# Performance work log

Measured on AMD Instinct MI355X. Metric: run time of the kernel, lower is better.

The kernel has to match this reference:

```python
import jax, jax.numpy as jnp
import numpy as np

EMBED_DIM = 1024
NUM_HEADS = 16
HEAD_DIM = EMBED_DIM // NUM_HEADS
B, S = 4, 2048


def setup_inputs() -> dict:
    key = jax.random.key(0)
    ks = jax.random.split(key, 9)
    scale = 1.0 / np.sqrt(EMBED_DIM)
    x = jax.random.normal(ks[0], (B, S, EMBED_DIM), dtype=jnp.float32)
    Wq = jax.random.uniform(ks[1], (EMBED_DIM, EMBED_DIM), jnp.float32, -scale, scale)
    bq = jax.random.uniform(ks[2], (EMBED_DIM,), jnp.float32, -scale, scale)
    Wk = jax.random.uniform(ks[3], (EMBED_DIM, EMBED_DIM), jnp.float32, -scale, scale)
    bk = jax.random.uniform(ks[4], (EMBED_DIM,), jnp.float32, -scale, scale)
    Wv = jax.random.uniform(ks[5], (EMBED_DIM, EMBED_DIM), jnp.float32, -scale, scale)
    bv = jax.random.uniform(ks[6], (EMBED_DIM,), jnp.float32, -scale, scale)
    Wo = jax.random.uniform(ks[7], (EMBED_DIM, EMBED_DIM), jnp.float32, -scale, scale)
    bo = jax.random.uniform(ks[8], (EMBED_DIM,), jnp.float32, -scale, scale)
    return {"x": x, "Wq": Wq, "bq": bq, "Wk": Wk, "bk": bk, "Wv": Wv, "bv": bv, "Wo": Wo, "bo": bo}


def reference(x, Wq, bq, Wk, bk, Wv, bv, Wo, bo):
    b, s, d = x.shape
    h, hd = NUM_HEADS, HEAD_DIM
    # projections -> [b, h, s, hd]
    def proj(W, bias):
        return (x @ W + bias).reshape(b, s, h, hd).transpose(0, 2, 1, 3)
    q = proj(Wq, bq)
    k = proj(Wk, bk)
    v = proj(Wv, bv)
    logits = jnp.einsum('bhqd,bhkd->bhqk', q, k) / np.sqrt(hd).astype(np.float32)
    attn = jax.nn.softmax(logits, axis=-1)  # dropout p=0.0 -> identity
    vals = jnp.einsum('bhqk,bhkd->bhqd', attn, v)
    vals = vals.transpose(0, 2, 1, 3).reshape(b, s, d)
    return vals @ Wo + bo
```

## Files before the change

### kernel.cpp

```cpp
#include <hip/hip_runtime.h>

typedef unsigned short u16;
typedef unsigned int u32;
typedef __bf16 bf16x8 __attribute__((ext_vector_type(8)));
typedef float f32x4 __attribute__((ext_vector_type(4)));
typedef float f32x16 __attribute__((ext_vector_type(16)));
typedef u32 u32x4 __attribute__((ext_vector_type(4)));
typedef u32 u32x2 __attribute__((ext_vector_type(2)));

#define NBATCH 4
#define NS 2048
#define ND 1024
#define NH 16
#define HDIM 64
#define KSCALE (0.125f * 1.44269504f)

#define MFMA(a, b, c) __builtin_amdgcn_mfma_f32_16x16x32_bf16(a, b, c, 0, 0, 0)
#define MFMA32(a, b, c) __builtin_amdgcn_mfma_f32_32x32x16_bf16(a, b, c, 0, 0, 0)

__device__ __forceinline__ u16 f2bf(float f) {
    u32 u = __builtin_bit_cast(u32, f);
    u += 0x7fffu + ((u >> 16) & 1u);
    return (u16)(u >> 16);
}

__device__ __forceinline__ u32 cvtpk(float a, float b) {
    u32 r;
    asm("v_cvt_pk_bf16_f32 %0, %1, %2" : "=v"(r) : "v"(a), "v"(b));
    return r;
}

__device__ __forceinline__ bf16x8 ldfrag(const u16* p) {
    u32x4 v = *(const u32x4*)p;
    return __builtin_bit_cast(bf16x8, v);
}

__device__ __forceinline__ void gld16(u16* lds, const u16* g) {
    __builtin_amdgcn_global_load_lds((__attribute__((address_space(1))) u32*)g,
                                     (__attribute__((address_space(3))) u32*)lds, 16, 0, 0);
}


__global__ __launch_bounds__(256) void prep(const float* __restrict__ x, const float* __restrict__ W0,
                                            const float* __restrict__ W1, const float* __restrict__ W2,
                                            const float* __restrict__ W3, u16* __restrict__ xb,
                                            u16* __restrict__ T0, u16* __restrict__ T1,
                                            u16* __restrict__ T2, u16* __restrict__ T3) {
    __shared__ u16 t[64][72];
    const int wg = blockIdx.x;
    const int tid = threadIdx.x;
    if (wg < 2048) {
        const int mt = wg >> 5, ktile = wg & 31;
        u16* out = xb + (size_t)wg * 4096;
#pragma unroll
        for (int half = 0; half < 2; ++half) {
            const int s = half * 256 + tid;
            const int rg = s >> 6, l = s & 63;
            const int row = mt * 128 + rg * 16 + (l & 15);
            const int col = ktile * 32 + (l >> 4) * 8;
            const float* sp = x + (size_t)row * ND + col;
            float4 v0 = *(const float4*)sp;
            float4 v1 = *(const float4*)(sp + 4);
            u32x4 o;
            o[0] = (u32)f2bf(v0.x) | ((u32)f2bf(v0.y) << 16);
            o[1] = (u32)f2bf(v0.z) | ((u32)f2bf(v0.w) << 16);
            o[2] = (u32)f2bf(v1.x) | ((u32)f2bf(v1.y) << 16);
            o[3] = (u32)f2bf(v1.z) | ((u32)f2bf(v1.w) << 16);
            *(u32x4*)(out + s * 8) = o;
        }
        return;
    }
    const int tt = wg - 2048;
    const int z = tt >> 8, r8 = tt & 255;
    const float* W = z == 0 ? W0 : z == 1 ? W1 : z == 2 ? W2 : W3;
    u16* WT = z == 0 ? T0 : z == 1 ? T1 : z == 2 ? T2 : T3;
    const int k0 = (r8 & 15) * 64, n0 = (r8 >> 4) * 64;
    {
        const int r = tid >> 2, cq = (tid & 3) * 16;
#pragma unroll
        for (int i = 0; i < 4; ++i) {
            float4 v = *(const float4*)(W + (size_t)(k0 + r) * ND + n0 + cq + i * 4);
            t[r][cq + i * 4 + 0] = f2bf(v.x);
            t[r][cq + i * 4 + 1] = f2bf(v.y);
            t[r][cq + i * 4 + 2] = f2bf(v.z);
            t[r][cq + i * 4 + 3] = f2bf(v.w);
        }
    }
    __syncthreads();
    {
        const int rr = tid >> 2, cq = (tid & 3) * 16;
        u32x4 o0, o1;
#pragma unroll
        for (int j = 0; j < 4; ++j) {
            o0[j] = (u32)t[cq + 2 * j][rr] | ((u32)t[cq + 2 * j + 1][rr] << 16);
            o1[j] = (u32)t[cq + 8 + 2 * j][rr] | ((u32)t[cq + 8 + 2 * j + 1][rr] << 16);
        }
        const int n_g = n0 + rr;
        const int nt = n_g >> 7, rgn = (n_g >> 4) & 7, lr = n_g & 15;
        const int k_g = k0 + cq;
        const int kt2 = k_g >> 5, lg = (k_g >> 3) & 3;
        u16* outb = WT + ((size_t)(nt * 32 + kt2)) * 4096 + rgn * 512 + lr * 8;
        *(u32x4*)(outb + lg * 128) = o0;
        *(u32x4*)(outb + (lg + 1) * 128) = o1;
    }
}

template <bool PF>
__device__ __forceinline__ void gemm_step(const bf16x8 (&a)[4], const bf16x8 (&b)[4],
                                          bf16x8 (&an)[4], bf16x8 (&bn)[4],
                                          const u16* aw, const u16* bw, int kt,
                                          f32x4 (&acc)[4][4]) {
    if (PF) {
        const u16* ap = aw + (size_t)(kt + 1) * 4096;
        const u16* bp = bw + (size_t)(kt + 1) * 4096;
#pragma unroll
        for (int i = 0; i < 4; ++i) {
            an[i] = ldfrag(ap + i * 512);
            bn[i] = ldfrag(bp + i * 512);
        }
    }
    __builtin_amdgcn_s_setprio(1);
#pragma unroll
    for (int mb = 0; mb < 4; ++mb)
#pragma unroll
        for (int nb = 0; nb < 4; ++nb)
            acc[mb][nb] = MFMA(a[mb], b[nb], acc[mb][nb]);
    __builtin_amdgcn_s_setprio(0);
}

__global__ __launch_bounds__(256, 3) void gemm_qkv(const u16* __restrict__ A,
                                                   const u16* __restrict__ wqT, const u16* __restrict__ wkT,
                                                   const u16* __restrict__ wvT,
                                                   const float* __restrict__ bq, const float* __restrict__ bk,
                                                   const float* __restrict__ bv,
                                                   u16* __restrict__ Qp, u16* __restrict__ Kf,
                                                   u16* __restrict__ Vf) {
    const int wg = blockIdx.x;
    const int xcd = wg & 7, idx = wg >> 3;
    const int ybl = xcd * 8 + idx / 24;
    const int xbl = idx % 24;
    const int region = xbl >> 3;
    const int m0 = ybl * 128, n0 = (xbl & 7) * 128;
    const u16* Bt = region == 0 ? wqT : region == 1 ? wkT : wvT;
    const float* bias = region == 0 ? bq : region == 1 ? bk : bv;

    const int tid = threadIdx.x;
    const int l = tid & 63, w = tid >> 6;
    const int lr = l & 15, lg = l >> 4;
    const int wr = w >> 1, wc = w & 1;

    const u16* aw = A + (size_t)ybl * 32 * 4096 + wr * 2048 + l * 8;
    const u16* bw = Bt + (size_t)(xbl & 7) * 32 * 4096 + wc * 2048 + l * 8;

    f32x4 acc[4][4] = {};
    bf16x8 aA[4], bA[4], aB[4], bB[4];
#pragma unroll
    for (int i = 0; i < 4; ++i) {
        aA[i] = ldfrag(aw + i * 512);
        bA[i] = ldfrag(bw + i * 512);
    }

    for (int kt = 0; kt < 32; kt += 2) {
        gemm_step<true>(aA, bA, aB, bB, aw, bw, kt, acc);
        if (kt + 2 < 32)
            gemm_step<true>(aB, bB, aA, bA, aw, bw, kt + 1, acc);
        else
            gemm_step<false>(aB, bB, aA, bA, aw, bw, kt + 1, acc);
    }

#pragma unroll
    for (int mb = 0; mb < 4; ++mb) {
#pragma unroll
        for (int nb = 0; nb < 4; ++nb) {
            const int col = n0 + wc * 64 + nb * 16 + lr;
            const float bia = bias[col];
            const int hd = col & 63, h = col >> 6;
            if (region == 2) {
                const int rowb = m0 + wr * 64 + mb * 16 + lg * 4;
                const int b = rowb >> 11, kv = rowb & 2047;
                const int bh = b * NH + h;
                const int ktp = kv >> 6, ks = (kv >> 4) & 3, hif = (kv >> 3) & 1, j0 = kv & 7;
                const int lane = (hd & 31) | (hif << 5);
                u32x2 o;
                o[0] = (u32)f2bf(acc[mb][nb][0] + bia) | ((u32)f2bf(acc[mb][nb][1] + bia) << 16);
                o[1] = (u32)f2bf(acc[mb][nb][2] + bia) | ((u32)f2bf(acc[mb][nb][3] + bia) << 16);
                size_t off = (size_t)bh * 131072 + (size_t)ktp * 4096 +
                             (size_t)(((ks + 4 * (hd >> 5)) * 64 + lane) * 8 + j0);
                *(u32x2*)(Vf + off) = o;
            } else if (region == 1) {
#pragma unroll
                for (int r = 0; r < 4; ++r) {
                    const int rowg = m0 + wr * 64 + mb * 16 + lg * 4 + r;
                    float v = (acc[mb][nb][r] + bia) * KSCALE;
                    const int b = rowg >> 11, kv = rowg & 2047;
                    const int bh = b * NH + h;
                    const int ktp = kv >> 6, kvb = (kv >> 5) & 1;
                    const int lane = (kv & 31) | (((hd >> 3) & 1) << 5);
                    size_t o = (size_t)bh * 131072 + (size_t)ktp * 4096 +
                               (size_t)(((kvb * 4 + (hd >> 4)) * 64 + lane) * 8 + (hd & 7));
                    Kf[o] = f2bf(v);
                }
            } else {
#pragma unroll
                for (int r = 0; r < 4; ++r) {
                    const int rowg = m0 + wr * 64 + mb * 16 + lg * 4 + r;
                    float v = acc[mb][nb][r] + bia;
                    size_t o = ((size_t)((rowg >> 11) * NH + h) * NS + (rowg & 2047)) * HDIM + hd;
                    Qp[o] = f2bf(v);
                }
            }
        }
    }
}

__global__ __launch_bounds__(256, 3) void gemm_o(const u16* __restrict__ A, const u16* __restrict__ Bt,
                                                 const float* __restrict__ bias, float* __restrict__ of32) {
    const int wg = blockIdx.x;
    const int xcd = wg & 7, idx = wg >> 3;
    const int ybl = xcd * 8 + (idx >> 3);
    const int xbl = idx & 7;
    const int m0 = ybl * 128, n0 = xbl * 128;

    const int tid = threadIdx.x;
    const int l = tid & 63, w = tid >> 6;
    const int lr = l & 15, lg = l >> 4;
    const int wr = w >> 1, wc = w & 1;

    const u16* aw = A + (size_t)ybl * 32 * 4096 + wr * 2048 + l * 8;
    const u16* bw = Bt + (size_t)xbl * 32 * 4096 + wc * 2048 + l * 8;

    f32x4 acc[4][4] = {};
    bf16x8 aA[4], bA[4], aB[4], bB[4];
#pragma unroll
    for (int i = 0; i < 4; ++i) {
        aA[i] = ldfrag(aw + i * 512);
        bA[i] = ldfrag(bw + i * 512);
    }

    for (int kt = 0; kt < 32; kt += 2) {
        gemm_step<true>(aA, bA, aB, bB, aw, bw, kt, acc);
        if (kt + 2 < 32)
            gemm_step<true>(aB, bB, aA, bA, aw, bw, kt + 1, acc);
        else
            gemm_step<false>(aB, bB, aA, bA, aw, bw, kt + 1, acc);
    }

#pragma unroll
    for (int mb = 0; mb < 4; ++mb) {
#pragma unroll
        for (int nb = 0; nb < 4; ++nb) {
            const int col = n0 + wc * 64 + nb * 16 + lr;
            const float bia = bias[col];
#pragma unroll
            for (int r = 0; r < 4; ++r) {
                const int rowg = m0 + wr * 64 + mb * 16 + lg * 4 + r;
                of32[(size_t)rowg * ND + col] = acc[mb][nb][r] + bia;
            }
        }
    }
}

__global__ __launch_bounds__(256, 3) void attn(const u16* __restrict__ Q, const u16* __restrict__ Kf,
                                               const u16* __restrict__ Vf, u16* __restrict__ AO) {
    __shared__ u16 sm[20480];
    const int tid = threadIdx.x;
    const int l = tid & 63, w = tid >> 6;
    const int lq = l & 31, hi = l >> 5;
    const int wg = blockIdx.x;
    const int xcd = wg & 7, idx = wg >> 3;
    const int bh = xcd * 8 + (idx >> 4);
    const int qb = idx & 15;
    const int qbase = qb * 128 + w * 32;

    const u16* Qrow = Q + ((size_t)bh * NS + qbase + lq) * HDIM;
    bf16x8 qf[4];
#pragma unroll
    for (int kh = 0; kh < 4; ++kh) qf[kh] = ldfrag(Qrow + kh * 16 + hi * 8);

    f32x16 oacc[2] = {};
    f32x16 sA[2] = {}, sB[2] = {};
    float ls0 = 0.f, ls1 = 0.f, ls2 = 0.f, ls3 = 0.f;

    const u16* KfB = Kf + (size_t)bh * 131072;
    const u16* VfB = Vf + (size_t)bh * 131072;

    auto finish = [&](f32x16(&prv)[2], const u16* vlb) {
#pragma unroll
        for (int kvb = 0; kvb < 2; ++kvb) {
#pragma unroll
            for (int i = 0; i < 16; i += 4) {
                float p0 = __builtin_amdgcn_exp2f(prv[kvb][i + 0]);
                float p1 = __builtin_amdgcn_exp2f(prv[kvb][i + 1]);
                float p2 = __builtin_amdgcn_exp2f(prv[kvb][i + 2]);
                float p3 = __builtin_amdgcn_exp2f(prv[kvb][i + 3]);
                prv[kvb][i + 0] = p0;
                prv[kvb][i + 1] = p1;
                prv[kvb][i + 2] = p2;
                prv[kvb][i + 3] = p3;
                ls0 += p0;
                ls1 += p1;
                ls2 += p2;
                ls3 += p3;
            }
        }
        bf16x8 pf[4];
#pragma unroll
        for (int ks = 0; ks < 4; ++ks) {
            const int i0 = 2 * ks, i1 = 2 * ks + 1;
            const int q20 = i0 & 3, kvb0 = i0 >> 2;
            const int q21 = i1 & 3, kvb1 = i1 >> 2;
            u32 W00 = cvtpk(prv[kvb0][4 * q20 + 0], prv[kvb0][4 * q20 + 1]);
            u32 W01 = cvtpk(prv[kvb0][4 * q20 + 2], prv[kvb0][4 * q20 + 3]);
            u32 W10 = cvtpk(prv[kvb1][4 * q21 + 0], prv[kvb1][4 * q21 + 1]);
            u32 W11 = cvtpk(prv[kvb1][4 * q21 + 2], prv[kvb1][4 * q21 + 3]);
            u32x2 s0 = __builtin_amdgcn_permlane32_swap(W00, W10, false, false);
            u32x2 s1 = __builtin_amdgcn_permlane32_swap(W01, W11, false, false);
            u32x4 words;
            words[0] = s0[0];
            words[1] = s1[0];
            words[2] = s0[1];
            words[3] = s1[1];
            pf[ks] = __builtin_bit_cast(bf16x8, words);
        }
#pragma unroll
        for (int hdb = 0; hdb < 2; ++hdb) {
            bf16x8 vf[4];
#pragma unroll
            for (int ks = 0; ks < 4; ++ks) vf[ks] = ldfrag(vlb + ((hdb * 4 + ks) * 64 + l) * 8);
            __builtin_amdgcn_s_setprio(1);
#pragma unroll
            for (int ks = 0; ks < 4; ++ks) oacc[hdb] = MFMA32(vf[ks], pf[ks], oacc[hdb]);
            __builtin_amdgcn_s_setprio(0);
        }
    };

    auto body = [&](int t, f32x16(&cur)[2], f32x16(&prv)[2], int dofin, int dostage) {
        if (dostage) {
            const u16* kg = KfB + (size_t)(t + 1) * 4096;
            const u16* vg = VfB + (size_t)(t + 1) * 4096;
            u16* kd = sm + ((t + 1) & 1) * 4096;
            u16* vd = sm + 8192 + ((t + 1) % 3) * 4096;
            gld16(kd + tid * 8, kg + tid * 8);
            gld16(kd + (256 + tid) * 8, kg + (256 + tid) * 8);
            gld16(vd + tid * 8, vg + tid * 8);
            gld16(vd + (256 + tid) * 8, vg + (256 + tid) * 8);
        }
        const u16* klb = sm + (t & 1) * 4096;
        f32x16 zv = {};
        cur[0] = zv;
        cur[1] = zv;
#pragma unroll
        for (int kvb = 0; kvb < 2; ++kvb) {
            bf16x8 kf[4];
#pragma unroll
            for (int kh = 0; kh < 4; ++kh) kf[kh] = ldfrag(klb + ((kvb * 4 + kh) * 64 + l) * 8);
            __builtin_amdgcn_s_setprio(1);
#pragma unroll
            for (int kh = 0; kh < 4; ++kh) cur[kvb] = MFMA32(kf[kh], qf[kh], cur[kvb]);
            __builtin_amdgcn_s_setprio(0);
        }
        if (dofin) finish(prv, sm + 8192 + ((t - 1) % 3) * 4096);
        __syncthreads();
    };

    gld16(sm + tid * 8, KfB + tid * 8);
    gld16(sm + (256 + tid) * 8, KfB + (256 + tid) * 8);
    gld16(sm + 8192 + tid * 8, VfB + tid * 8);
    gld16(sm + 8192 + (256 + tid) * 8, VfB + (256 + tid) * 8);
    __syncthreads();

    body(0, sA, sB, 0, 1);
    for (int t = 1; t < 31; t += 2) {
        body(t, sB, sA, 1, 1);
        body(t + 1, sA, sB, 1, 1);
    }
    body(31, sB, sA, 1, 0);
    finish(sB, sm + 8192 + (31 % 3) * 4096);

    float lsum = (ls0 + ls1) + (ls2 + ls3);
    lsum += __shfl_xor(lsum, 32);

    u16* ot = sm + w * 2048;
    const float inv = 1.f / lsum;
#pragma unroll
    for (int hdb = 0; hdb < 2; ++hdb)
#pragma unroll
        for (int q2 = 0; q2 < 4; ++q2)
#pragma unroll
            for (int rp = 0; rp < 2; ++rp) {
                u32 word = cvtpk(oacc[hdb][4 * q2 + 2 * rp] * inv, oacc[hdb][4 * q2 + 2 * rp + 1] * inv);
                const int hd0 = hdb * 32 + 8 * q2 + 4 * hi + 2 * rp;
                const int byteoff = lq * 128 + ((2 * hd0) ^ ((lq & 7) << 4));
                *(u32*)((char*)ot + byteoff) = word;
            }
    const int b = bh >> 4, h = bh & 15;
#pragma unroll
    for (int p = 0; p < 4; ++p) {
        const int pidx = p * 64 + l;
        const int row = pidx >> 3;
        const int cb = ((pidx & 7) * 16) ^ ((row & 7) << 4);
        u32x4 val = *(u32x4*)((char*)ot + row * 128 + cb);
        const int m = b * NS + qbase + row;
        const int c = h * 64 + (pidx & 7) * 8;
        const int mt = m >> 7, rg = (m >> 4) & 7, lrm = m & 15;
        const int ktile = c >> 5, lgc = (c >> 3) & 3;
        *(u32x4*)(AO + ((size_t)(mt * 32 + ktile)) * 4096 + rg * 512 + (lgc * 16 + lrm) * 8) = val;
    }
}

extern "C" void kernel_launch(void* const* d_in, const int* in_sizes, int n_in,
                              void* d_out, int out_size, void* d_ws, size_t ws_size,
                              hipStream_t stream) {
    const float* x = (const float*)d_in[0];
    const float* Wq = (const float*)d_in[1];
    const float* bq = (const float*)d_in[2];
    const float* Wk = (const float*)d_in[3];
    const float* bk = (const float*)d_in[4];
    const float* Wv = (const float*)d_in[5];
    const float* bv = (const float*)d_in[6];
    const float* Wo = (const float*)d_in[7];
    const float* bo = (const float*)d_in[8];
    float* out = (float*)d_out;

    u16* ws = (u16*)d_ws;
    u16* xb = ws;
    u16* wqT = ws + 8388608;
    u16* wkT = wqT + 1048576;
    u16* wvT = wkT + 1048576;
    u16* woT = wvT + 1048576;
    u16* Qp = woT + 1048576;
    u16* Kfp = Qp + 8388608;
    u16* Vfp = Kfp + 8388608;
    u16* AO = xb;

    prep<<<3072, 256, 0, stream>>>(x, Wq, Wk, Wv, Wo, xb, wqT, wkT, wvT, woT);
    gemm_qkv<<<1536, 256, 0, stream>>>(xb, wqT, wkT, wvT, bq, bk, bv, Qp, Kfp, Vfp);
    attn<<<1024, 256, 0, stream>>>(Qp, Kfp, Vfp, AO);
    gemm_o<<<512, 256, 0, stream>>>(AO, woT, bo, out);
}
```

Measured before the change: 183.5 us.

## Drop cross-tile software pipelining in attention to raise occupancy to 4 waves

Removes the two-stage S/P pipeline, which kept two score-accumulator sets live across KV tiles, and instead computes scores, exp, packing and the PV MFMA within each KV sub-block. V staging shrinks from triple to double buffering, reducing LDS from 40KB to 32KB, and launch bounds rise from 3 to 4 blocks per CU. The aim is to lower register and LDS pressure so more waves can hide latency. The cost is less intra-wave overlap between the exp/convert work and the MFMA work.

Result: no change. 183.5 us (median of 2 runs) (+0.0%).

```diff
diff --git a/kernel.cpp b/kernel.cpp
--- a/kernel.cpp
+++ b/kernel.cpp
@@ -260,9 +260,9 @@
     }
 }
 
-__global__ __launch_bounds__(256, 3) void attn(const u16* __restrict__ Q, const u16* __restrict__ Kf,
+__global__ __launch_bounds__(256, 4) void attn(const u16* __restrict__ Q, const u16* __restrict__ Kf,
                                                const u16* __restrict__ Vf, u16* __restrict__ AO) {
-    __shared__ u16 sm[20480];
+    __shared__ u16 sm[16384];
     const int tid = threadIdx.x;
     const int l = tid & 63, w = tid >> 6;
     const int lq = l & 31, hi = l >> 5;
@@ -278,90 +278,10 @@
     for (int kh = 0; kh < 4; ++kh) qf[kh] = ldfrag(Qrow + kh * 16 + hi * 8);
 
     f32x16 oacc[2] = {};
-    f32x16 sA[2] = {}, sB[2] = {};
     float ls0 = 0.f, ls1 = 0.f, ls2 = 0.f, ls3 = 0.f;
 
     const u16* KfB = Kf + (size_t)bh * 131072;
     const u16* VfB = Vf + (size_t)bh * 131072;
-
-    auto finish = [&](f32x16(&prv)[2], const u16* vlb) {
-#pragma unroll
-        for (int kvb = 0; kvb < 2; ++kvb) {
-#pragma unroll
-            for (int i = 0; i < 16; i += 4) {
-                float p0 = __builtin_amdgcn_exp2f(prv[kvb][i + 0]);
-                float p1 = __builtin_amdgcn_exp2f(prv[kvb][i + 1]);
-                float p2 = __builtin_amdgcn_exp2f(prv[kvb][i + 2]);
-                float p3 = __builtin_amdgcn_exp2f(prv[kvb][i + 3]);
-                prv[kvb][i + 0] = p0;
-                prv[kvb][i + 1] = p1;
-                prv[kvb][i + 2] = p2;
-                prv[kvb][i + 3] = p3;
-                ls0 += p0;
-                ls1 += p1;
-                ls2 += p2;
-                ls3 += p3;
-            }
-        }
-        bf16x8 pf[4];
-#pragma unroll
-        for (int ks = 0; ks < 4; ++ks) {
-            const int i0 = 2 * ks, i1 = 2 * ks + 1;
-            const int q20 = i0 & 3, kvb0 = i0 >> 2;
-            const int q21 = i1 & 3, kvb1 = i1 >> 2;
-            u32 W00 = cvtpk(prv[kvb0][4 * q20 + 0], prv[kvb0][4 * q20 + 1]);
-            u32 W01 = cvtpk(prv[kvb0][4 * q20 + 2], prv[kvb0][4 * q20 + 3]);
-            u32 W10 = cvtpk(prv[kvb1][4 * q21 + 0], prv[kvb1][4 * q21 + 1]);
-            u32 W11 = cvtpk(prv[kvb1][4 * q21 + 2], prv[kvb1][4 * q21 + 3]);
-            u32x2 s0 = __builtin_amdgcn_permlane32_swap(W00, W10, false, false);
-            u32x2 s1 = __builtin_amdgcn_permlane32_swap(W01, W11, false, false);
-            u32x4 words;
-            words[0] = s0[0];
-            words[1] = s1[0];
-            words[2] = s0[1];
-            words[3] = s1[1];
-            pf[ks] = __builtin_bit_cast(bf16x8, words);
-        }
-#pragma unroll
-        for (int hdb = 0; hdb < 2; ++hdb) {
-            bf16x8 vf[4];
-#pragma unroll
-            for (int ks = 0; ks < 4; ++ks) vf[ks] = ldfrag(vlb + ((hdb * 4 + ks) * 64 + l) * 8);
-            __builtin_amdgcn_s_setprio(1);
-#pragma unroll
-            for (int ks = 0; ks < 4; ++ks) oacc[hdb] = MFMA32(vf[ks], pf[ks], oacc[hdb]);
-            __builtin_amdgcn_s_setprio(0);
-        }
-    };
-
-    auto body = [&](int t, f32x16(&cur)[2], f32x16(&prv)[2], int dofin, int dostage) {
-        if (dostage) {
-            const u16* kg = KfB + (size_t)(t + 1) * 4096;
-            const u16* vg = VfB + (size_t)(t + 1) * 4096;
-            u16* kd = sm + ((t + 1) & 1) * 4096;
-            u16* vd = sm + 8192 + ((t + 1) % 3) * 4096;
-            gld16(kd + tid * 8, kg + tid * 8);
-            gld16(kd + (256 + tid) * 8, kg + (256 + tid) * 8);
-            gld16(vd + tid * 8, vg + tid * 8);
-            gld16(vd + (256 + tid) * 8, vg + (256 + tid) * 8);
-        }
-        const u16* klb = sm + (t & 1) * 4096;
-        f32x16 zv = {};
-        cur[0] = zv;
-        cur[1] = zv;
-#pragma unroll
-        for (int kvb = 0; kvb < 2; ++kvb) {
-            bf16x8 kf[4];
-#pragma unroll
-            for (int kh = 0; kh < 4; ++kh) kf[kh] = ldfrag(klb + ((kvb * 4 + kh) * 64 + l) * 8);
-            __builtin_amdgcn_s_setprio(1);
-#pragma unroll
-            for (int kh = 0; kh < 4; ++kh) cur[kvb] = MFMA32(kf[kh], qf[kh], cur[kvb]);
-            __builtin_amdgcn_s_setprio(0);
-        }
-        if (dofin) finish(prv, sm + 8192 + ((t - 1) % 3) * 4096);
-        __syncthreads();
-    };
 
     gld16(sm + tid * 8, KfB + tid * 8);
     gld16(sm + (256 + tid) * 8, KfB + (256 + tid) * 8);
@@ -369,13 +289,93 @@
     gld16(sm + 8192 + (256 + tid) * 8, VfB + (256 + tid) * 8);
     __syncthreads();
 
-    body(0, sA, sB, 0, 1);
-    for (int t = 1; t < 31; t += 2) {
-        body(t, sB, sA, 1, 1);
-        body(t + 1, sA, sB, 1, 1);
-    }
-    body(31, sB, sA, 1, 0);
-    finish(sB, sm + 8192 + (31 % 3) * 4096);
+    for (int kt = 0; kt < 32; ++kt) {
+        const int cur = kt & 1;
+        if (kt < 31) {
+            const u16* kg = KfB + (size_t)(kt + 1) * 4096;
+            const u16* vg = VfB + (size_t)(kt + 1) * 4096;
+            u16* kd = sm + (cur ^ 1) * 4096;
+            u16* vd = sm + 8192 + (cur ^ 1) * 4096;
+            gld16(kd + tid * 8, kg + tid * 8);
+            gld16(kd + (256 + tid) * 8, kg + (256 + tid) * 8);
+            gld16(vd + tid * 8, vg + tid * 8);
+            gld16(vd + (256 + tid) * 8, vg + (256 + tid) * 8);
+        }
+        const u16* klb = sm + cur * 4096;
+        const u16* vlb = sm + 8192 + cur * 4096;
+
+#pragma unroll
+        for (int kvb = 0; kvb < 2; ++kvb) {
+            bf16x8 kf[4];
+#pragma unroll
+            for (int kh = 0; kh < 4; ++kh)
+                kf[kh] = ldfrag(klb + ((kvb * 4 + kh) * 64 + l) * 8);
+
+            f32x16 sacc = {};
+            __builtin_amdgcn_s_setprio(1);
+#pragma unroll
+            for (int kh = 0; kh < 4; ++kh) sacc = MFMA32(kf[kh], qf[kh], sacc);
+            __builtin_amdgcn_s_setprio(0);
+
+#pragma unroll
+            for (int i = 0; i < 16; i += 4) {
+                float p0 = __builtin_amdgcn_exp2f(sacc[i + 0]);
+                float p1 = __builtin_amdgcn_exp2f(sacc[i + 1]);
+                float p2 = __builtin_amdgcn_exp2f(sacc[i + 2]);
+                float p3 = __builtin_amdgcn_exp2f(sacc[i + 3]);
+                sacc[i + 0] = p0;
+                sacc[i + 1] = p1;
+                sacc[i + 2] = p2;
+                sacc[i + 3] = p3;
+                ls0 += p0;
+                ls1 += p1;
+                ls2 += p2;
+                ls3 += p3;
+            }
+
+            bf16x8 pf0, pf1;
+            {
+                u32 W00 = cvtpk(sacc[0], sacc[1]);
+                u32 W01 = cvtpk(sacc[2], sacc[3]);
+                u32 W10 = cvtpk(sacc[4], sacc[5]);
+                u32 W11 = cvtpk(sacc[6], sacc[7]);
+                u32x2 s0 = __builtin_amdgcn_permlane32_swap(W00, W10, false, false);
+                u32x2 s1 = __builtin_amdgcn_permlane32_swap(W01, W11, false, false);
+                u32x4 words;
+                words[0] = s0[0];
+                words[1] = s1[0];
+                words[2] = s0[1];
+                words[3] = s1[1];
+                pf0 = __builtin_bit_cast(bf16x8, words);
+            }
+            {
+                u32 W00 = cvtpk(sacc[8], sacc[9]);
+                u32 W01 = cvtpk(sacc[10], sacc[11]);
+                u32 W10 = cvtpk(sacc[12], sacc[13]);
+                u32 W11 = cvtpk(sacc[14], sacc[15]);
+                u32x2 s0 = __builtin_amdgcn_permlane32_swap(W00, W10, false, false);
+                u32x2 s1 = __builtin_amdgcn_permlane32_swap(W01, W11, false, false);
+                u32x4 words;
+                words[0] = s0[0];
+                words[1] = s1[0];
+                words[2] = s0[1];
+                words[3] = s1[1];
+                pf1 = __builtin_bit_cast(bf16x8, words);
+            }
+
+#pragma unroll
+            for (int hdb = 0; hdb < 2; ++hdb) {
+                bf16x8 vf0 = ldfrag(vlb + ((hdb * 4 + kvb * 2 + 0) * 64 + l) * 8);
+                bf16x8 vf1 = ldfrag(vlb + ((hdb * 4 + kvb * 2 + 1) * 64 + l) * 8);
+                __builtin_amdgcn_s_setprio(1);
+                oacc[hdb] = MFMA32(vf0, pf0, oacc[hdb]);
+                oacc[hdb] = MFMA32(vf1, pf1, oacc[hdb]);
+                __builtin_amdgcn_s_setprio(0);
+            }
+        }
+
+        __syncthreads();
+    }
 
     float lsum = (ls0 + ls1) + (ls2 + ls3);
     lsum += __shfl_xor(lsum, 32);
```
